# Kernel optimization log

Measured on AMD Instinct MI355X. Metric: run time of the kernel, lower is better.

Reference implementation:

```python
import jax, jax.numpy as jnp
import numpy as np

# dims
B, L, HID, TDIM, LT = 8, 4096, 1024, 768, 77
DIM = 512            # vmamba_dim
D_INNER = 2 * DIM    # expand = 2
NHEADS = DIM // 16   # 32
HEADDIM = D_INNER // NHEADS  # 32
D_STATE = 64
CONV_K = 4
CONV_DIM = D_INNER + 2 * D_STATE  # 1152
D_PROJ = 2 * D_INNER + 2 * D_STATE + NHEADS  # z | xBC | dt


def setup_inputs() -> dict:
    key = jax.random.key(0)
    ks = jax.random.split(key, 20)
    s = 0.02
    return {
        "image_tokens": jax.random.normal(ks[0], (B, L, HID), jnp.float32),
        "text_tokens": jax.random.normal(ks[1], (B, LT, TDIM), jnp.float32),
        "W_in": jax.random.normal(ks[2], (HID, DIM), jnp.float32) * s,
        "b_in": jnp.zeros((DIM,), jnp.float32),
        "W_txt": jax.random.normal(ks[3], (TDIM, DIM), jnp.float32) * s,
        "b_txt": jnp.zeros((DIM,), jnp.float32),
        "norm_w": jnp.ones((DIM,), jnp.float32),
        "norm_b": jnp.zeros((DIM,), jnp.float32),
        "W_zxbcdt": jax.random.normal(ks[4], (DIM, D_PROJ), jnp.float32) * s,
        "b_zxbcdt": jnp.zeros((D_PROJ,), jnp.float32),
        "conv_w": jax.random.normal(ks[5], (CONV_DIM, CONV_K), jnp.float32) * 0.1,
        "conv_b": jnp.zeros((CONV_DIM,), jnp.float32),
        "dt_bias": jax.random.uniform(ks[6], (NHEADS,), jnp.float32, -4.0, -2.0),
        "A_log": jnp.log(jnp.arange(1, NHEADS + 1, dtype=jnp.float32)),
        "D": jnp.ones((NHEADS,), jnp.float32),
        "W_blk_out": jax.random.normal(ks[7], (D_INNER, DIM), jnp.float32) * s,
        "b_blk_out": jnp.zeros((DIM,), jnp.float32),
        "W_out": jax.random.normal(ks[8], (DIM, HID), jnp.float32) * s,
        "b_out": jnp.zeros((HID,), jnp.float32),
    }


def _layernorm(x, w, b, eps=1e-5):
    mu = x.mean(-1, keepdims=True)
    var = ((x - mu) ** 2).mean(-1, keepdims=True)
    return (x - mu) * jax.lax.rsqrt(var + eps) * w + b


def _mamba2_block(tok, norm_w, norm_b, W_zxbcdt, b_zxbcdt, conv_w, conv_b,
                  dt_bias, A_log, Dp, W_blk_out, b_blk_out):
    x = _layernorm(tok, norm_w, norm_b)
    zxbcdt = x @ W_zxbcdt + b_zxbcdt                       # [B,L,D_PROJ]
    z = zxbcdt[..., :D_INNER]
    xBC = zxbcdt[..., D_INNER:D_INNER + CONV_DIM]
    dt = zxbcdt[..., D_INNER + CONV_DIM:]                  # [B,L,H]
    # causal depthwise conv1d, kernel 4
    xp = jnp.pad(xBC, ((0, 0), (CONV_K - 1, 0), (0, 0)))
    conv = sum(xp[:, k:k + L, :] * conv_w[None, None, :, k] for k in range(CONV_K))
    xBC = jax.nn.silu(conv + conv_b)
    xh = xBC[..., :D_INNER].reshape(B, L, NHEADS, HEADDIM)  # [B,L,H,P]
    Bm = xBC[..., D_INNER:D_INNER + D_STATE]                # [B,L,N]
    Cm = xBC[..., D_INNER + D_STATE:]                       # [B,L,N]
    dt = jax.nn.softplus(dt + dt_bias)                      # [B,L,H]
    A = -jnp.exp(A_log)                                     # [H]
    dA = jnp.exp(dt * A)                                    # [B,L,H]

    def step(h, xs):
        dA_t, dt_t, B_t, C_t, x_t = xs   # [B,H],[B,H],[B,N],[B,N],[B,H,P]
        h = h * dA_t[:, :, None, None] + \
            (dt_t[:, :, None, None] * x_t[..., None]) * B_t[:, None, None, :]
        y = jnp.einsum('bhpn,bn->bhp', h, C_t)
        return h, y

    xs = (dA.transpose(1, 0, 2), dt.transpose(1, 0, 2),
          Bm.transpose(1, 0, 2), Cm.transpose(1, 0, 2),
          xh.transpose(1, 0, 2, 3))
    h0 = jnp.zeros((B, NHEADS, HEADDIM, D_STATE), tok.dtype)
    _, ys = jax.lax.scan(step, h0, xs)                      # [L,B,H,P]
    y = ys.transpose(1, 0, 2, 3) + Dp[None, None, :, None] * xh
    y = y.reshape(B, L, D_INNER) * jax.nn.silu(z)
    return tok + (y @ W_blk_out + b_blk_out)                # residual


def reference(image_tokens, text_tokens, W_in, b_in, W_txt, b_txt,
              norm_w, norm_b, W_zxbcdt, b_zxbcdt, conv_w, conv_b,
              dt_bias, A_log, D, W_blk_out, b_blk_out, W_out, b_out):
    txt = text_tokens[:, 0, :] @ W_txt + b_txt              # cls pool
    tok = image_tokens @ W_in + b_in + txt[:, None, :]
    tok = _mamba2_block(tok, norm_w, norm_b, W_zxbcdt, b_zxbcdt, conv_w,
                        conv_b, dt_bias, A_log, D, W_blk_out, b_blk_out)
    tok = tok @ W_out + b_out                               # [B,L,HID]
    return tok.mean(axis=1)                                 # AdaptiveAvgPool1d(1)
```

## Files before the change

kernel.cpp:

```cpp
#include <hip/hip_runtime.h>

typedef unsigned short U16;
typedef __attribute__((ext_vector_type(2))) float f32x2;
typedef __attribute__((ext_vector_type(4))) float f32x4;
typedef __attribute__((ext_vector_type(8))) short short8;
typedef __attribute__((ext_vector_type(8))) __bf16 bf16x8;

#define Bsz 8
#define Lsz 4096
#define HID 1024
#define DIMV 512
#define D_INNER 1024
#define NHEADS 32
#define HEADDIM 32
#define D_STATE 64
#define CONV_DIM 1152
#define D_PROJ 2208
#define D_PROJ_PAD 2304
#define MROWS 32768
#define CL2 512
#define NSUB 8
#define NCH 8

__device__ __forceinline__ float bf2f(U16 u) {
  return __builtin_bit_cast(float, (unsigned)(((unsigned)u) << 16));
}
__device__ __forceinline__ U16 f2bf(float f) {
  unsigned u = __builtin_bit_cast(unsigned, f);
  return (U16)((u + 0x7FFFu + ((u >> 16) & 1u)) >> 16);
}
__device__ __forceinline__ void gload_lds16(const void* g, void* l) {
  __builtin_amdgcn_global_load_lds((const __attribute__((address_space(1))) unsigned int*)g,
                                   (__attribute__((address_space(3))) unsigned int*)l, 16, 0, 0);
}

__global__ __launch_bounds__(512) void txt_kernel(const float* __restrict__ text,
                                                  const float* __restrict__ Wt,
                                                  const float* __restrict__ bt,
                                                  float* __restrict__ txt) {
  int b = blockIdx.x, j = threadIdx.x;
  float s = bt[j];
  const float* tp = text + (size_t)b * 77 * 768;
  for (int k = 0; k < 768; ++k) s += tp[k] * Wt[(size_t)k * 512 + j];
  txt[b * 512 + j] = s;
}

__global__ __launch_bounds__(256) void transpose_cvt_kernel(const float* __restrict__ in,
                                                            U16* __restrict__ out,
                                                            int K, int N, int Npad) {
  __shared__ U16 tile[32][33];
  int n0 = blockIdx.x * 32, k0 = blockIdx.y * 32;
  int tx = threadIdx.x, ty = threadIdx.y;
  #pragma unroll
  for (int i = 0; i < 4; ++i) {
    int k = k0 + ty + i * 8, n = n0 + tx;
    float v = (n < N) ? in[(size_t)k * N + n] : 0.f;
    tile[ty + i * 8][tx] = f2bf(v);
  }
  __syncthreads();
  #pragma unroll
  for (int i = 0; i < 4; ++i) {
    int n = n0 + ty + i * 8;
    out[(size_t)n * K + k0 + tx] = tile[tx][ty + i * 8];
  }
}

template <int EPI, int AF32>
__global__ __launch_bounds__(256) void gemm_kernel(const void* __restrict__ Ap,
                                                   const U16* __restrict__ Bt,
                                                   U16* __restrict__ C,
                                                   const float* __restrict__ bias,
                                                   const float* __restrict__ txtv,
                                                   int M, int K, int Nreal) {
  __shared__ alignas(16) U16 As[128 * 64];
  __shared__ alignas(16) U16 Bs[128 * 64];
  const int tid = threadIdx.x;
  const int wid = tid >> 6, lane = tid & 63;
  const int lhi = lane >> 4, llo = lane & 15;
  const int m0 = blockIdx.x * 128;
  const int n0 = blockIdx.y * 128;
  const int wr = wid >> 1, wc = wid & 1;
  f32x4 acc[4][4] = {};

  for (int k0 = 0; k0 < K; k0 += 64) {
    __syncthreads();
    if constexpr (AF32) {
      const float* Af = (const float*)Ap;
      #pragma unroll
      for (int is = 0; is < 4; ++is) {
        int q = is * 256 + tid;
        int r = q >> 3, cl = q & 7;
        int cg = cl ^ (r & 7);
        const float* src = Af + (size_t)(m0 + r) * K + k0 + cg * 8;
        f32x4 v0 = *reinterpret_cast<const f32x4*>(src);
        f32x4 v1 = *reinterpret_cast<const f32x4*>(src + 4);
        short8 o;
        #pragma unroll
        for (int j = 0; j < 4; ++j) {
          o[j] = (short)f2bf(v0[j]);
          o[j + 4] = (short)f2bf(v1[j]);
        }
        *reinterpret_cast<short8*>(&As[q * 8]) = o;
      }
    } else {
      const U16* A = (const U16*)Ap;
      #pragma unroll
      for (int is = 0; is < 4; ++is) {
        int qbase = is * 256 + wid * 64;
        int q = qbase + lane;
        int r = q >> 3;
        int cc = (q & 7) ^ (r & 7);
        gload_lds16(A + (size_t)(m0 + r) * K + k0 + cc * 8, &As[qbase * 8]);
      }
    }
    #pragma unroll
    for (int is = 0; is < 4; ++is) {
      int qbase = is * 256 + wid * 64;
      int q = qbase + lane;
      int r = q >> 3;
      int cc = (q & 7) ^ (r & 7);
      gload_lds16(Bt + (size_t)(n0 + r) * K + k0 + cc * 8, &Bs[qbase * 8]);
    }
    __syncthreads();
    #pragma unroll
    for (int kk = 0; kk < 64; kk += 32) {
      bf16x8 av[4], bv[4];
      #pragma unroll
      for (int i = 0; i < 4; ++i) {
        int ra = wr * 64 + i * 16 + llo;
        short8 a = *reinterpret_cast<const short8*>(
            &As[ra * 64 + ((((kk >> 3) + lhi) ^ (ra & 7)) << 3)]);
        av[i] = __builtin_bit_cast(bf16x8, a);
        int rb = wc * 64 + i * 16 + llo;
        short8 b = *reinterpret_cast<const short8*>(
            &Bs[rb * 64 + ((((kk >> 3) + lhi) ^ (rb & 7)) << 3)]);
        bv[i] = __builtin_bit_cast(bf16x8, b);
      }
      #pragma unroll
      for (int i = 0; i < 4; ++i)
        #pragma unroll
        for (int j = 0; j < 4; ++j)
          acc[i][j] = __builtin_amdgcn_mfma_f32_16x16x32_bf16(av[i], bv[j], acc[i][j], 0, 0, 0);
    }
  }
  const int b = m0 >> 12;
  #pragma unroll
  for (int i = 0; i < 4; ++i) {
    int rbase = m0 + wr * 64 + i * 16 + lhi * 4;
    #pragma unroll
    for (int j = 0; j < 4; ++j) {
      int cg = n0 + wc * 64 + j * 16 + llo;
      if (cg < Nreal) {
        float badd = bias[cg] + (EPI ? txtv[b * 512 + cg] : 0.f);
        #pragma unroll
        for (int r = 0; r < 4; ++r)
          C[(size_t)(rbase + r) * Nreal + cg] = f2bf(acc[i][j][r] + badd);
      }
    }
  }
}

__global__ __launch_bounds__(128) void ln_kernel(const U16* __restrict__ tok,
                                                 U16* __restrict__ xo,
                                                 const float* __restrict__ w,
                                                 const float* __restrict__ bb) {
  int row = blockIdx.x, tid = threadIdx.x;
  const U16* rp = tok + (size_t)row * 512 + tid * 4;
  uint2 raw = *reinterpret_cast<const uint2*>(rp);
  float f0 = bf2f((U16)(raw.x & 0xffff)), f1 = bf2f((U16)(raw.x >> 16));
  float f2 = bf2f((U16)(raw.y & 0xffff)), f3 = bf2f((U16)(raw.y >> 16));
  float s = f0 + f1 + f2 + f3;
  float q = f0 * f0 + f1 * f1 + f2 * f2 + f3 * f3;
  for (int m = 1; m < 64; m <<= 1) { s += __shfl_xor(s, m); q += __shfl_xor(q, m); }
  __shared__ float ss[2], qq[2];
  if ((tid & 63) == 0) { ss[tid >> 6] = s; qq[tid >> 6] = q; }
  __syncthreads();
  s = ss[0] + ss[1]; q = qq[0] + qq[1];
  float mu = s * (1.f / 512.f);
  float var = q * (1.f / 512.f) - mu * mu;
  float rs = rsqrtf(var + 1e-5f);
  int j0 = tid * 4;
  unsigned c0 = f2bf((f0 - mu) * rs * w[j0] + bb[j0]);
  unsigned c1 = f2bf((f1 - mu) * rs * w[j0 + 1] + bb[j0 + 1]);
  unsigned c2 = f2bf((f2 - mu) * rs * w[j0 + 2] + bb[j0 + 2]);
  unsigned c3 = f2bf((f3 - mu) * rs * w[j0 + 3] + bb[j0 + 3]);
  uint2 o; o.x = c0 | (c1 << 16); o.y = c2 | (c3 << 16);
  *reinterpret_cast<uint2*>(xo + (size_t)row * 512 + j0) = o;
}

__global__ __launch_bounds__(256) void tokpart_kernel(const U16* __restrict__ tok,
                                                      float* __restrict__ part) {
  int b = blockIdx.x, j = blockIdx.y * 256 + threadIdx.x, z = blockIdx.z;
  float s = 0.f;
  int l0 = z * 256;
  for (int l = l0; l < l0 + 256; ++l)
    s += bf2f(tok[((size_t)b * Lsz + l) * 512 + j]);
  part[(z * 8 + b) * 512 + j] = s;
}

__global__ __launch_bounds__(256) void decay_kernel(const U16* __restrict__ zx,
                                                    const float* __restrict__ dt_bias,
                                                    const float* __restrict__ A_log,
                                                    float* __restrict__ decay4) {
  const int sc = blockIdx.x;
  const int w = threadIdx.x >> 6, l = threadIdx.x & 63;
  const int r0 = sc * 64;
  const int b = r0 >> 12, l0 = r0 & 4095;
  #pragma unroll
  for (int i = 0; i < 8; ++i) {
    int hh = w * 8 + i;
    float raw = bf2f(zx[(size_t)(r0 + l) * D_PROJ + 2176 + hh]) + dt_bias[hh];
    float dt = (raw > 20.f) ? raw : log1pf(__expf(raw));
    float A = -__expf(A_log[hh]);
    float ldA2 = dt * A * 1.44269504088896f;
    float ldt2 = __log2f(dt);
    float la = ldA2;
    #pragma unroll
    for (int d = 1; d < 64; d <<= 1) {
      float o = __shfl_up(la, d);
      if (l >= d) la += o;
    }
    float laend = __shfl(la, 63);
    f32x4 v = {ldt2 - la, la, exp2f(la), exp2f(laend + ldt2 - la)};
    *reinterpret_cast<f32x4*>(decay4 + ((size_t)(b * 32 + hh) * 4096 + l0 + l) * 4) = v;
  }
}

__global__ __launch_bounds__(256) void conv_tr_kernel(
    const U16* __restrict__ zx, const float* __restrict__ cw,
    const float* __restrict__ cb, U16* __restrict__ Bmo, U16* __restrict__ Cmo,
    U16* __restrict__ xh_t, U16* __restrict__ gz_t,
    U16* __restrict__ bm_t, U16* __restrict__ cm_t) {
  __shared__ U16 tile[64 * 72];
  const int lt = blockIdx.x, ct = blockIdx.y;
  const int r0 = lt * 64;
  const int b = r0 >> 12, l0 = r0 & 4095;
  const int tid = threadIdx.x;
  const int c = tid & 63, lqb = tid >> 6;

  if (ct < 16) {
    const int zc0 = ct * 64;
    #pragma unroll
    for (int it = 0; it < 4; ++it) {
      int lq4 = (lqb + it * 4) * 4;
      float v[4];
      #pragma unroll
      for (int j = 0; j < 4; ++j) {
        float z = bf2f(zx[(size_t)(r0 + lq4 + j) * D_PROJ + zc0 + c]);
        v[j] = z / (1.f + __expf(-z));
      }
      uint2 p2;
      p2.x = (unsigned)f2bf(v[0]) | ((unsigned)f2bf(v[1]) << 16);
      p2.y = (unsigned)f2bf(v[2]) | ((unsigned)f2bf(v[3]) << 16);
      *reinterpret_cast<uint2*>(reinterpret_cast<char*>(tile) + (size_t)c * 144 + lq4 * 2) = p2;
    }
    __syncthreads();
    int c2 = tid >> 2, seg = tid & 3;
    const char* src = reinterpret_cast<const char*>(tile) + (size_t)c2 * 144 + seg * 32;
    f32x4 a = *reinterpret_cast<const f32x4*>(src);
    f32x4 bq = *reinterpret_cast<const f32x4*>(src + 16);
    U16* dst = gz_t + ((size_t)b * 1024 + zc0 + c2) * 4096 + l0 + seg * 16;
    *reinterpret_cast<f32x4*>(dst) = a;
    *reinterpret_cast<f32x4*>(dst + 8) = bq;
  } else {
    const int cc = (ct - 16) * 64 + c;
    const float4 w4 = *reinterpret_cast<const float4*>(cw + cc * 4);
    const float cbv = cb[cc];
    #pragma unroll
    for (int it = 0; it < 4; ++it) {
      int lq4 = (lqb + it * 4) * 4;
      float v7[7];
      #pragma unroll
      for (int k = 0; k < 7; ++k) {
        int lrel = lq4 + k - 3;
        v7[k] = (l0 + lrel >= 0)
                    ? bf2f(zx[(size_t)(r0 + lrel) * D_PROJ + D_INNER + cc])
                    : 0.f;
      }
      float o[4];
      #pragma unroll
      for (int j = 0; j < 4; ++j) {
        float acc = cbv + v7[j] * w4.x + v7[j + 1] * w4.y + v7[j + 2] * w4.z + v7[j + 3] * w4.w;
        o[j] = acc / (1.f + __expf(-acc));
      }
      uint2 p2;
      p2.x = (unsigned)f2bf(o[0]) | ((unsigned)f2bf(o[1]) << 16);
      p2.y = (unsigned)f2bf(o[2]) | ((unsigned)f2bf(o[3]) << 16);
      *reinterpret_cast<uint2*>(reinterpret_cast<char*>(tile) + (size_t)c * 144 + lq4 * 2) = p2;
      if (cc >= 1024) {
        U16* outp = (cc < 1088) ? Bmo : Cmo;
        int n = cc & 63;
        #pragma unroll
        for (int j = 0; j < 4; ++j)
          outp[(size_t)(r0 + lq4 + j) * 64 + n] = f2bf(o[j]);
      }
    }
    __syncthreads();
    int c2 = tid >> 2, seg = tid & 3;
    const char* src = reinterpret_cast<const char*>(tile) + (size_t)c2 * 144 + seg * 32;
    f32x4 a = *reinterpret_cast<const f32x4*>(src);
    f32x4 bq = *reinterpret_cast<const f32x4*>(src + 16);
    int cc2 = (ct - 16) * 64 + c2;
    U16* dst;
    if (cc2 < 1024)      dst = xh_t + ((size_t)b * 1024 + cc2) * 4096 + l0 + seg * 16;
    else if (cc2 < 1088) dst = bm_t + ((size_t)(b * 64 + cc2 - 1024)) * 4096 + l0 + seg * 16;
    else                 dst = cm_t + ((size_t)(b * 64 + cc2 - 1088)) * 4096 + l0 + seg * 16;
    *reinterpret_cast<f32x4*>(dst) = a;
    *reinterpret_cast<f32x4*>(dst + 8) = bq;
  }
}

__global__ __launch_bounds__(256, 2) void scan_chunk_kernel(
    const U16* __restrict__ xh_t, const U16* __restrict__ gz_t,
    const U16* __restrict__ Bm, const U16* __restrict__ Cm,
    const U16* __restrict__ bm_t, const U16* __restrict__ cm_t,
    const float* __restrict__ decay4, const float* __restrict__ Dp,
    float* __restrict__ hpart, float* __restrict__ wacc,
    float* __restrict__ ylocal, float* __restrict__ aprod) {
  const int w = threadIdx.x >> 6, l = threadIdx.x & 63;
  const int u = blockIdx.x * 4 + w;
  const int hh = u & 31, ci = (u >> 5) & 7, b = u >> 8;
  const int tl = l & 15, lg = l >> 4;

  __shared__ alignas(16) U16 MsmAll[4 * 64 * 72];
  __shared__ alignas(16) float decAll[4 * 256];
  U16* Msm = &MsmAll[w * 64 * 72];
  float* qsm = &decAll[w * 256];
  float* la2sm = qsm + 64;
  float* casm = qsm + 128;
  float* cfsm = qsm + 192;

  #pragma unroll
  for (int i = 0; i < 9; ++i)
    *reinterpret_cast<f32x4*>(reinterpret_cast<char*>(Msm) + (size_t)l * 144 + i * 16) =
        f32x4{0.f, 0.f, 0.f, 0.f};

  f32x4 hC[2][4] = {};
  f32x4 WB[2][4] = {};
  float corrv[2][4] = {};
  float ylac[2] = {0.f, 0.f}, dxac[2] = {0.f, 0.f};
  float capfx = 1.f;
  const size_t xgrow = ((size_t)b * 1024 + hh * 32) * 4096;
  const float* dbase = decay4 + ((size_t)(b * 32 + hh) * 4096) * 4;

  for (int sc = 0; sc < NSUB; ++sc) {
    const int lglob = ci * CL2 + sc * 64;
    const int r0g = b * 4096 + lglob;

    f32x4 dv = *reinterpret_cast<const f32x4*>(dbase + (size_t)(lglob + l) * 4);
    qsm[l] = dv[0];
    la2sm[l] = dv[1];
    casm[l] = dv[2];
    cfsm[l] = dv[3];

    f32x4 g[10];
    #pragma unroll
    for (int i = 0; i < 10; ++i) g[i] = f32x4{0.f, 0.f, 0.f, 0.f};
    #pragma unroll
    for (int k = 0; k < 2; ++k) {
      bf16x8 af[4], cf4[4];
      #pragma unroll
      for (int si = 0; si < 4; ++si)
        af[si] = *reinterpret_cast<const bf16x8*>(
            Bm + (size_t)(r0g + si * 16 + tl) * 64 + k * 32 + lg * 8);
      #pragma unroll
      for (int ti = 0; ti < 4; ++ti)
        cf4[ti] = *reinterpret_cast<const bf16x8*>(
            Cm + (size_t)(r0g + ti * 16 + tl) * 64 + k * 32 + lg * 8);
      int idx = 0;
      #pragma unroll
      for (int si = 0; si < 4; ++si)
        #pragma unroll
        for (int ti = si; ti < 4; ++ti) {
          g[idx] = __builtin_amdgcn_mfma_f32_16x16x32_bf16(af[si], cf4[ti], g[idx], 0, 0, 0);
          ++idx;
        }
    }

    {
      int idx = 0;
      #pragma unroll
      for (int si = 0; si < 4; ++si) {
        f32x4 q4 = *reinterpret_cast<const f32x4*>(&qsm[si * 16 + lg * 4]);
        #pragma unroll
        for (int ti = si; ti < 4; ++ti) {
          float lat = la2sm[ti * 16 + tl];
          f32x4 gv = g[idx]; ++idx;
          float v[4];
          #pragma unroll
          for (int r = 0; r < 4; ++r) {
            float val = gv[r] * exp2f(lat + q4[r]);
            if (si == ti) val = (lg * 4 + r <= tl) ? val : 0.f;
            v[r] = val;
          }
          uint2 pk;
          pk.x = (unsigned)f2bf(v[0]) | ((unsigned)f2bf(v[1]) << 16);
          pk.y = (unsigned)f2bf(v[2]) | ((unsigned)f2bf(v[3]) << 16);
          *reinterpret_cast<uint2*>(reinterpret_cast<char*>(Msm) +
                                    (size_t)(ti * 16 + tl) * 144 + (size_t)(si * 16 + lg * 4) * 2) = pk;
        }
      }
    }

    {
      bf16x8 xb[2][2];
      #pragma unroll
      for (int pt = 0; pt < 2; ++pt)
        #pragma unroll
        for (int ks = 0; ks < 2; ++ks)
          xb[pt][ks] = *reinterpret_cast<const bf16x8*>(
              xh_t + xgrow + (size_t)(pt * 16 + tl) * 4096 + lglob + ks * 32 + lg * 8);
      #pragma unroll
      for (int tt = 0; tt < 4; ++tt) {
        f32x4 y[2] = {f32x4{0.f, 0.f, 0.f, 0.f}, f32x4{0.f, 0.f, 0.f, 0.f}};
        #pragma unroll
        for (int ks = 0; ks < 2; ++ks) {
          bf16x8 mf = *reinterpret_cast<const bf16x8*>(
              reinterpret_cast<char*>(Msm) + (size_t)(tt * 16 + tl) * 144 + (ks * 32 + lg * 8) * 2);
          #pragma unroll
          for (int pt = 0; pt < 2; ++pt)
            y[pt] = __builtin_amdgcn_mfma_f32_16x16x32_bf16(mf, xb[pt][ks], y[pt], 0, 0, 0);
        }
        #pragma unroll
        for (int pt = 0; pt < 2; ++pt) {
          size_t ro = xgrow + (size_t)(pt * 16 + tl) * 4096 + lglob + tt * 16 + lg * 4;
          uint2 gz2 = *reinterpret_cast<const uint2*>(gz_t + ro);
          uint2 xx2 = *reinterpret_cast<const uint2*>(xh_t + ro);
          float gzv[4] = {bf2f((U16)(gz2.x & 0xffff)), bf2f((U16)(gz2.x >> 16)),
                          bf2f((U16)(gz2.y & 0xffff)), bf2f((U16)(gz2.y >> 16))};
          float xxv[4] = {bf2f((U16)(xx2.x & 0xffff)), bf2f((U16)(xx2.x >> 16)),
                          bf2f((U16)(xx2.y & 0xffff)), bf2f((U16)(xx2.y >> 16))};
          #pragma unroll
          for (int r = 0; r < 4; ++r) {
            ylac[pt] = fmaf(gzv[r], y[pt][r], ylac[pt]);
            dxac[pt] = fmaf(gzv[r], xxv[r], dxac[pt]);
          }
        }
      }
    }

    bf16x8 ga[2][2], xa[2][2];
    #pragma unroll
    for (int pt = 0; pt < 2; ++pt)
      #pragma unroll
      for (int kt = 0; kt < 2; ++kt) {
        size_t ro = xgrow + (size_t)(pt * 16 + tl) * 4096 + lglob + kt * 32 + lg * 8;
        short8 graw = *reinterpret_cast<const short8*>(gz_t + ro);
        short8 xraw = *reinterpret_cast<const short8*>(xh_t + ro);
        const float* cap = &casm[kt * 32 + lg * 8];
        const float* cfp = &cfsm[kt * 32 + lg * 8];
        short8 gs, xs8;
        #pragma unroll
        for (int j = 0; j < 8; ++j) {
          gs[j] = (short)f2bf(bf2f((U16)graw[j]) * cap[j]);
          xs8[j] = (short)f2bf(bf2f((U16)xraw[j]) * cfp[j]);
        }
        ga[pt][kt] = __builtin_bit_cast(bf16x8, gs);
        xa[pt][kt] = __builtin_bit_cast(bf16x8, xs8);
      }
    f32x4 ws[2][4] = {};
    f32x4 hs[2][4] = {};
    #pragma unroll
    for (int kt = 0; kt < 2; ++kt) {
      bf16x8 cbf[4], bbf[4];
      #pragma unroll
      for (int nt = 0; nt < 4; ++nt) {
        cbf[nt] = *reinterpret_cast<const bf16x8*>(
            cm_t + (size_t)(b * 64 + nt * 16 + tl) * 4096 + lglob + kt * 32 + lg * 8);
        bbf[nt] = *reinterpret_cast<const bf16x8*>(
            bm_t + (size_t)(b * 64 + nt * 16 + tl) * 4096 + lglob + kt * 32 + lg * 8);
      }
      #pragma unroll
      for (int pt = 0; pt < 2; ++pt)
        #pragma unroll
        for (int nt = 0; nt < 4; ++nt) {
          ws[pt][nt] = __builtin_amdgcn_mfma_f32_16x16x32_bf16(ga[pt][kt], cbf[nt], ws[pt][nt], 0, 0, 0);
          hs[pt][nt] = __builtin_amdgcn_mfma_f32_16x16x32_bf16(xa[pt][kt], bbf[nt], hs[pt][nt], 0, 0, 0);
        }
    }

    float cs = casm[63];
    #pragma unroll
    for (int pt = 0; pt < 2; ++pt) {
      f32x4 a4 = hC[pt][0] * ws[pt][0] + hC[pt][1] * ws[pt][1] +
                 hC[pt][2] * ws[pt][2] + hC[pt][3] * ws[pt][3];
      #pragma unroll
      for (int r = 0; r < 4; ++r) {
        float cc = a4[r];
        cc += __shfl_xor(cc, 1); cc += __shfl_xor(cc, 2);
        cc += __shfl_xor(cc, 4); cc += __shfl_xor(cc, 8);
        corrv[pt][r] += cc;
      }
      #pragma unroll
      for (int nt = 0; nt < 4; ++nt) {
        WB[pt][nt] = WB[pt][nt] + ws[pt][nt] * capfx;
        hC[pt][nt] = hC[pt][nt] * cs + hs[pt][nt];
      }
    }
    capfx *= cs;
  }

  #pragma unroll
  for (int pt = 0; pt < 2; ++pt)
    #pragma unroll
    for (int nt = 0; nt < 4; ++nt) {
      size_t slot = (size_t)u * 2048 + (size_t)((pt * 4 + nt) * 64 + l) * 4;
      *reinterpret_cast<f32x4*>(hpart + slot) = hC[pt][nt];
      *reinterpret_cast<f32x4*>(wacc + slot) = WB[pt][nt];
    }
  const float Dh = Dp[hh];
  float* ysm = qsm;
  #pragma unroll
  for (int pt = 0; pt < 2; ++pt) {
    float yv = ylac[pt] + Dh * dxac[pt];
    yv += __shfl_xor(yv, 16);
    yv += __shfl_xor(yv, 32);
    if (l < 16) ysm[pt * 16 + l] = yv;
  }
  if (tl == 0) {
    #pragma unroll
    for (int pt = 0; pt < 2; ++pt)
      #pragma unroll
      for (int r = 0; r < 4; ++r)
        ysm[pt * 16 + lg * 4 + r] += corrv[pt][r];
  }
  if (l < 32) ylocal[(size_t)u * 32 + l] = ysm[l];
  if (l == 0) aprod[u] = capfx;
}

__global__ __launch_bounds__(64) void scan_combine_kernel(
    const float* __restrict__ hpart, const float* __restrict__ wacc,
    const float* __restrict__ ylocal, const float* __restrict__ aprod,
    float* __restrict__ yysum) {
  const int bh = blockIdx.x;
  const int b = bh >> 5, hh = bh & 31;
  const int l = threadIdx.x, tl = l & 15, lg = l >> 4;
  __shared__ float ysm[32];
  f32x4 hr[8] = {};
  float cv[8] = {};
  float ylsum = 0.f;
  for (int ci = 0; ci < NCH; ++ci) {
    int bx = (b * NCH + ci) * 32 + hh;
    size_t base = (size_t)bx * 2048 + (size_t)l * 4;
    f32x4 w[8], p[8];
    #pragma unroll
    for (int t8 = 0; t8 < 8; ++t8) {
      w[t8] = *reinterpret_cast<const f32x4*>(wacc + base + t8 * 256);
      p[t8] = *reinterpret_cast<const f32x4*>(hpart + base + t8 * 256);
    }
    float ap = aprod[bx];
    #pragma unroll
    for (int pt = 0; pt < 2; ++pt) {
      f32x4 a4 = hr[pt * 4] * w[pt * 4] + hr[pt * 4 + 1] * w[pt * 4 + 1] +
                 hr[pt * 4 + 2] * w[pt * 4 + 2] + hr[pt * 4 + 3] * w[pt * 4 + 3];
      #pragma unroll
      for (int r = 0; r < 4; ++r) cv[pt * 4 + r] += a4[r];
    }
    #pragma unroll
    for (int t8 = 0; t8 < 8; ++t8) hr[t8] = hr[t8] * ap + p[t8];
    if (l < 32) ylsum += ylocal[(size_t)bx * 32 + l];
  }
  #pragma unroll
  for (int i = 0; i < 8; ++i) {
    cv[i] += __shfl_xor(cv[i], 1); cv[i] += __shfl_xor(cv[i], 2);
    cv[i] += __shfl_xor(cv[i], 4); cv[i] += __shfl_xor(cv[i], 8);
  }
  if (l < 32) ysm[l] = ylsum;
  __syncthreads();
  if (tl == 0) {
    #pragma unroll
    for (int pt = 0; pt < 2; ++pt)
      #pragma unroll
      for (int r = 0; r < 4; ++r)
        ysm[pt * 16 + lg * 4 + r] += cv[pt * 4 + r];
  }
  __syncthreads();
  if (l < 32) yysum[(size_t)b * 1024 + hh * 32 + l] = ysm[l];
}

__global__ __launch_bounds__(128) void final1_kernel(const float* __restrict__ tokpart,
                                                     const float* __restrict__ yysum,
                                                     const float* __restrict__ Wb,
                                                     const float* __restrict__ bb,
                                                     float* __restrict__ m2) {
  int b = blockIdx.x, j = blockIdx.y * 128 + threadIdx.x;
  float tm = 0.f;
  #pragma unroll
  for (int z = 0; z < 16; ++z) tm += tokpart[(z * 8 + b) * 512 + j];
  float s = 0.f;
  for (int d = 0; d < 1024; ++d) s += yysum[b * 1024 + d] * Wb[(size_t)d * 512 + j];
  m2[b * 512 + j] = (tm + s) * (1.f / (float)Lsz) + bb[j];
}

__global__ __launch_bounds__(256) void final2_kernel(const float* __restrict__ m2,
                                                     const float* __restrict__ Wo,
                                                     const float* __restrict__ bo,
                                                     float* __restrict__ out) {
  int b = blockIdx.x, o = blockIdx.y * 256 + threadIdx.x;
  float s = 0.f;
  for (int j = 0; j < 512; ++j) s += m2[b * 512 + j] * Wo[(size_t)j * 1024 + o];
  out[b * 1024 + o] = s + bo[o];
}

extern "C" void kernel_launch(void* const* d_in, const int* in_sizes, int n_in,
                              void* d_out, int out_size, void* d_ws, size_t ws_size,
                              hipStream_t stream) {
  const float* image = (const float*)d_in[0];
  const float* text = (const float*)d_in[1];
  const float* W_in = (const float*)d_in[2];
  const float* b_in = (const float*)d_in[3];
  const float* W_txt = (const float*)d_in[4];
  const float* b_txt = (const float*)d_in[5];
  const float* norm_w = (const float*)d_in[6];
  const float* norm_b = (const float*)d_in[7];
  const float* W_zx = (const float*)d_in[8];
  const float* b_zx = (const float*)d_in[9];
  const float* conv_w = (const float*)d_in[10];
  const float* conv_b = (const float*)d_in[11];
  const float* dt_bias = (const float*)d_in[12];
  const float* A_log = (const float*)d_in[13];
  const float* Dp = (const float*)d_in[14];
  const float* W_blk = (const float*)d_in[15];
  const float* b_blk = (const float*)d_in[16];
  const float* W_out = (const float*)d_in[17];
  const float* b_out = (const float*)d_in[18];
  float* out = (float*)d_out;

  char* ws = (char*)d_ws;
  size_t off = 0;
  auto take = [&](size_t bytes) {
    char* p = ws + off;
    off = (off + bytes + 255) & ~(size_t)255;
    return p;
  };
  U16* gz_t = (U16*)take((size_t)MROWS * HID * 2);
  U16* wt_in = (U16*)take((size_t)DIMV * HID * 2);
  U16* wt_zx = (U16*)take((size_t)D_PROJ_PAD * DIMV * 2);
  U16* tok_bf = (U16*)take((size_t)MROWS * DIMV * 2);
  U16* x_bf = (U16*)take((size_t)MROWS * DIMV * 2);
  U16* zx_bf = (U16*)take((size_t)MROWS * D_PROJ * 2);
  U16* xh_t = (U16*)take((size_t)MROWS * D_INNER * 2);
  U16* bm_bf = (U16*)take((size_t)MROWS * 64 * 2);
  U16* cm_bf = (U16*)take((size_t)MROWS * 64 * 2);
  U16* bm_t = (U16*)take((size_t)MROWS * 64 * 2);
  U16* cm_t = (U16*)take((size_t)MROWS * 64 * 2);
  float* decay4 = (float*)take((size_t)256 * 4096 * 16);
  float* txtf = (float*)take(8 * 512 * 4);
  float* tokpart = (float*)take(16 * 8 * 512 * 4);
  float* yysum = (float*)take(8 * 1024 * 4);
  float* m2 = (float*)take(8 * 512 * 4);
  float* ylocal = (float*)take((size_t)2048 * 32 * 4);
  float* aprod = (float*)take((size_t)2048 * 4);
  float* hpart = (float*)tok_bf;
  float* wacc = (float*)x_bf;

  txt_kernel<<<8, 512, 0, stream>>>(text, W_txt, b_txt, txtf);
  transpose_cvt_kernel<<<dim3(DIMV / 32, HID / 32), dim3(32, 8), 0, stream>>>(W_in, wt_in, HID, DIMV, DIMV);
  transpose_cvt_kernel<<<dim3(D_PROJ_PAD / 32, DIMV / 32), dim3(32, 8), 0, stream>>>(W_zx, wt_zx, DIMV, D_PROJ, D_PROJ_PAD);

  gemm_kernel<1, 1><<<dim3(MROWS / 128, DIMV / 128), 256, 0, stream>>>(
      (const void*)image, wt_in, tok_bf, b_in, txtf, MROWS, HID, DIMV);
  tokpart_kernel<<<dim3(8, 2, 16), 256, 0, stream>>>(tok_bf, tokpart);
  ln_kernel<<<MROWS, 128, 0, stream>>>(tok_bf, x_bf, norm_w, norm_b);

  gemm_kernel<0, 0><<<dim3(MROWS / 128, D_PROJ_PAD / 128), 256, 0, stream>>>(
      (const void*)x_bf, wt_zx, zx_bf, b_zx, nullptr, MROWS, DIMV, D_PROJ);

  decay_kernel<<<512, 256, 0, stream>>>(zx_bf, dt_bias, A_log, decay4);
  conv_tr_kernel<<<dim3(MROWS / 64, 34), 256, 0, stream>>>(zx_bf, conv_w, conv_b, bm_bf, cm_bf,
                                                           xh_t, gz_t, bm_t, cm_t);

  scan_chunk_kernel<<<512, 256, 0, stream>>>(xh_t, gz_t, bm_bf, cm_bf, bm_t, cm_t,
                                             decay4, Dp, hpart, wacc, ylocal, aprod);
  scan_combine_kernel<<<256, 64, 0, stream>>>(hpart, wacc, ylocal, aprod, yysum);

  final1_kernel<<<dim3(8, 4), 128, 0, stream>>>(tokpart, yysum, W_blk, b_blk, m2);
  final2_kernel<<<dim3(8, 4), 256, 0, stream>>>(m2, W_out, b_out, out);
}
```

Baseline: 640.6 us.

## Split scan into 16 chunks, swizzle block order, widen combine kernel

Halves the scan chunk length (CL2 512→256, NSUB 8→4) and doubles the number of chunks to 16, so scan_chunk launches 1024 blocks instead of 512 and gets more parallelism. Block indices are swizzled across groups of 8 so that neighbouring blocks touch different batches and chunks. The combine kernel now uses 4 waves, each handling two state slices, with an LDS reduction, to cover the longer sequential combine over 16 chunks. The trade-off is more partial-state traffic (hpart/wacc) and a longer serial carry chain in the combine step. hpart and wacc still alias tok_bf and x_bf, which are large enough to hold the doubled partials.

```diff
diff --git a/kernel.cpp b/kernel.cpp
--- a/kernel.cpp
+++ b/kernel.cpp
@@ -18,9 +18,9 @@
 #define D_PROJ 2208
 #define D_PROJ_PAD 2304
 #define MROWS 32768
-#define CL2 512
-#define NSUB 8
-#define NCH 8
+#define CL2 256
+#define NSUB 4
+#define NCH 16
 
 __device__ __forceinline__ float bf2f(U16 u) {
   return __builtin_bit_cast(float, (unsigned)(((unsigned)u) << 16));
@@ -318,8 +318,9 @@
     float* __restrict__ hpart, float* __restrict__ wacc,
     float* __restrict__ ylocal, float* __restrict__ aprod) {
   const int w = threadIdx.x >> 6, l = threadIdx.x & 63;
-  const int u = blockIdx.x * 4 + w;
-  const int hh = u & 31, ci = (u >> 5) & 7, b = u >> 8;
+  const int bid = (blockIdx.x & 7) * 128 + (blockIdx.x >> 3);
+  const int u = bid * 4 + w;
+  const int hh = u & 31, ci = (u >> 5) & (NCH - 1), b = u >> 9;
   const int tl = l & 15, lg = l >> 4;
 
   __shared__ alignas(16) U16 MsmAll[4 * 64 * 72];
@@ -528,54 +529,57 @@
   if (l == 0) aprod[u] = capfx;
 }
 
-__global__ __launch_bounds__(64) void scan_combine_kernel(
+__global__ __launch_bounds__(256) void scan_combine_kernel(
     const float* __restrict__ hpart, const float* __restrict__ wacc,
     const float* __restrict__ ylocal, const float* __restrict__ aprod,
     float* __restrict__ yysum) {
   const int bh = blockIdx.x;
   const int b = bh >> 5, hh = bh & 31;
-  const int l = threadIdx.x, tl = l & 15, lg = l >> 4;
-  __shared__ float ysm[32];
-  f32x4 hr[8] = {};
-  float cv[8] = {};
-  float ylsum = 0.f;
+  const int w = threadIdx.x >> 6, l = threadIdx.x & 63;
+  const int tl = l & 15, lg = l >> 4;
+  __shared__ float csm[8][16];
+  __shared__ float ylsm[32];
+  const int pair0 = w * 2;
+  f32x4 hr[2] = {};
+  float cv[2][4] = {};
   for (int ci = 0; ci < NCH; ++ci) {
     int bx = (b * NCH + ci) * 32 + hh;
     size_t base = (size_t)bx * 2048 + (size_t)l * 4;
-    f32x4 w[8], p[8];
-    #pragma unroll
-    for (int t8 = 0; t8 < 8; ++t8) {
-      w[t8] = *reinterpret_cast<const f32x4*>(wacc + base + t8 * 256);
-      p[t8] = *reinterpret_cast<const f32x4*>(hpart + base + t8 * 256);
-    }
     float ap = aprod[bx];
     #pragma unroll
-    for (int pt = 0; pt < 2; ++pt) {
-      f32x4 a4 = hr[pt * 4] * w[pt * 4] + hr[pt * 4 + 1] * w[pt * 4 + 1] +
-                 hr[pt * 4 + 2] * w[pt * 4 + 2] + hr[pt * 4 + 3] * w[pt * 4 + 3];
-      #pragma unroll
-      for (int r = 0; r < 4; ++r) cv[pt * 4 + r] += a4[r];
-    }
-    #pragma unroll
-    for (int t8 = 0; t8 < 8; ++t8) hr[t8] = hr[t8] * ap + p[t8];
-    if (l < 32) ylsum += ylocal[(size_t)bx * 32 + l];
-  }
-  #pragma unroll
-  for (int i = 0; i < 8; ++i) {
-    cv[i] += __shfl_xor(cv[i], 1); cv[i] += __shfl_xor(cv[i], 2);
-    cv[i] += __shfl_xor(cv[i], 4); cv[i] += __shfl_xor(cv[i], 8);
-  }
-  if (l < 32) ysm[l] = ylsum;
+    for (int k = 0; k < 2; ++k) {
+      size_t o = base + (size_t)(pair0 + k) * 256;
+      f32x4 wv = *reinterpret_cast<const f32x4*>(wacc + o);
+      f32x4 pv = *reinterpret_cast<const f32x4*>(hpart + o);
+      f32x4 a4 = hr[k] * wv;
+      #pragma unroll
+      for (int r = 0; r < 4; ++r) cv[k][r] += a4[r];
+      hr[k] = hr[k] * ap + pv;
+    }
+  }
+  #pragma unroll
+  for (int k = 0; k < 2; ++k)
+    #pragma unroll
+    for (int r = 0; r < 4; ++r) {
+      float c = cv[k][r];
+      c += __shfl_xor(c, 1); c += __shfl_xor(c, 2);
+      c += __shfl_xor(c, 4); c += __shfl_xor(c, 8);
+      if (tl == 0) csm[pair0 + k][lg * 4 + r] = c;
+    }
+  if (threadIdx.x < 32) {
+    float yl = 0.f;
+    for (int ci = 0; ci < NCH; ++ci)
+      yl += ylocal[(size_t)((b * NCH + ci) * 32 + hh) * 32 + threadIdx.x];
+    ylsm[threadIdx.x] = yl;
+  }
   __syncthreads();
-  if (tl == 0) {
-    #pragma unroll
-    for (int pt = 0; pt < 2; ++pt)
-      #pragma unroll
-      for (int r = 0; r < 4; ++r)
-        ysm[pt * 16 + lg * 4 + r] += cv[pt * 4 + r];
-  }
-  __syncthreads();
-  if (l < 32) yysum[(size_t)b * 1024 + hh * 32 + l] = ysm[l];
+  if (threadIdx.x < 32) {
+    int p = threadIdx.x;
+    int pt = p >> 4, pl = p & 15;
+    float corr = csm[pt * 4 + 0][pl] + csm[pt * 4 + 1][pl] +
+                 csm[pt * 4 + 2][pl] + csm[pt * 4 + 3][pl];
+    yysum[(size_t)b * 1024 + hh * 32 + p] = ylsm[p] + corr;
+  }
 }
 
 __global__ __launch_bounds__(128) void final1_kernel(const float* __restrict__ tokpart,
@@ -649,8 +653,8 @@
   float* tokpart = (float*)take(16 * 8 * 512 * 4);
   float* yysum = (float*)take(8 * 1024 * 4);
   float* m2 = (float*)take(8 * 512 * 4);
-  float* ylocal = (float*)take((size_t)2048 * 32 * 4);
-  float* aprod = (float*)take((size_t)2048 * 4);
+  float* ylocal = (float*)take((size_t)4096 * 32 * 4);
+  float* aprod = (float*)take((size_t)4096 * 4);
   float* hpart = (float*)tok_bf;
   float* wacc = (float*)x_bf;
 
@@ -670,9 +674,9 @@
   conv_tr_kernel<<<dim3(MROWS / 64, 34), 256, 0, stream>>>(zx_bf, conv_w, conv_b, bm_bf, cm_bf,
                                                            xh_t, gz_t, bm_t, cm_t);
 
-  scan_chunk_kernel<<<512, 256, 0, stream>>>(xh_t, gz_t, bm_bf, cm_bf, bm_t, cm_t,
-                                             decay4, Dp, hpart, wacc, ylocal, aprod);
-  scan_combine_kernel<<<256, 64, 0, stream>>>(hpart, wacc, ylocal, aprod, yysum);
+  scan_chunk_kernel<<<1024, 256, 0, stream>>>(xh_t, gz_t, bm_bf, cm_bf, bm_t, cm_t,
+                                              decay4, Dp, hpart, wacc, ylocal, aprod);
+  scan_combine_kernel<<<256, 256, 0, stream>>>(hpart, wacc, ylocal, aprod, yysum);
 
   final1_kernel<<<dim3(8, 4), 128, 0, stream>>>(tokpart, yysum, W_blk, b_blk, m2);
   final2_kernel<<<dim3(8, 4), 256, 0, stream>>>(m2, W_out, b_out, out);
```

New measurement: 657.2 us. 1.03x slower.
